# Performance work log

Measured on AMD Instinct MI355X. Metric: run time of the kernel, lower is better.

## Reference

```python
import jax, jax.numpy as jnp
import numpy as np

N_NODES = 50000
N_EDGES = 800000
F = 64
R = 32


def setup_inputs() -> dict:
    key = jax.random.key(0)
    ks = jax.random.split(key, 12)
    s = jax.random.normal(ks[0], (N_NODES, F), dtype=jnp.float32)
    v = jax.random.normal(ks[1], (N_NODES, 3, F), dtype=jnp.float32)
    radial_embeddings = jax.random.normal(ks[2], (N_EDGES, R), dtype=jnp.float32)
    f_cut = jax.random.uniform(ks[3], (N_EDGES,), dtype=jnp.float32)
    unit_vectors = jax.random.normal(ks[4], (N_EDGES, 3), dtype=jnp.float32)
    edge_index = jax.random.randint(ks[5], (2, N_EDGES), 0, N_NODES, dtype=jnp.int64 if jax.config.jax_enable_x64 else jnp.int32)
    # mlp_phi: Linear(F,F) -> SiLU -> Linear(F, 3F); linear_W: Linear(R, 3F)
    W1 = jax.random.normal(ks[6], (F, F), dtype=jnp.float32) / np.sqrt(F)
    b1 = jnp.zeros((F,), dtype=jnp.float32)
    W2 = jax.random.normal(ks[7], (F, 3 * F), dtype=jnp.float32) / np.sqrt(F)
    b2 = jnp.zeros((3 * F,), dtype=jnp.float32)
    Wr = jax.random.normal(ks[8], (R, 3 * F), dtype=jnp.float32) / np.sqrt(R)
    br = jnp.zeros((3 * F,), dtype=jnp.float32)
    return {"s": s, "v": v, "radial_embeddings": radial_embeddings, "f_cut": f_cut,
            "unit_vectors": unit_vectors, "edge_index": edge_index,
            "W1": W1, "b1": b1, "W2": W2, "b2": b2, "Wr": Wr, "br": br}


def reference(s, v, radial_embeddings, f_cut, unit_vectors, edge_index, W1, b1, W2, b2, Wr, br):
    idx_i, idx_j = edge_index[0], edge_index[1]
    n_nodes = s.shape[0]
    nf = s.shape[-1]
    # per-node MLP: Linear -> SiLU -> Linear to 3F channels
    phi = jax.nn.silu(s @ W1 + b1) @ W2 + b2            # [N, 3F]
    # radial filter weighted by cutoff
    W = (radial_embeddings @ Wr + br) * f_cut[:, None]   # [E, 3F]
    x = phi[idx_j] * W                                   # [E, 3F]  (gather + multiply)
    x_s, x_vv, x_vs = x[:, :nf], x[:, nf:2 * nf], x[:, 2 * nf:]
    ds = jax.ops.segment_sum(x_s, idx_i, num_segments=n_nodes)          # [N, F]
    x_v = v[idx_j] * x_vv[:, None, :] + x_vs[:, None, :] * unit_vectors[:, :, None]  # [E, 3, F]
    dv = jax.ops.segment_sum(x_v, idx_i, num_segments=n_nodes)          # [N, 3, F]
    return s + ds, v + dv
```

## Files before the change

kernel.cpp:

```cpp
#include <hip/hip_runtime.h>
#include <math.h>

#define N_NODES 50000
#define N_EDGES 800000
#define F 64
#define R 32
#define C3F 192
#define CAP 48
#define CSTRIDE 16
#define MLP_BLOCKS ((N_NODES + 31) / 32)
#define FILL_BLOCKS ((N_EDGES + 255) / 256)

#define REP32(X) X(0) X(1) X(2) X(3) X(4) X(5) X(6) X(7) \
                 X(8) X(9) X(10) X(11) X(12) X(13) X(14) X(15) \
                 X(16) X(17) X(18) X(19) X(20) X(21) X(22) X(23) \
                 X(24) X(25) X(26) X(27) X(28) X(29) X(30) X(31)

__global__ __launch_bounds__(256) void mlp_fill_kernel(
    const float* __restrict__ s, const float* __restrict__ W1,
    const float* __restrict__ b1, const float* __restrict__ W2,
    const float* __restrict__ b2, float* __restrict__ phi,
    const int* __restrict__ eidx, int* __restrict__ counts,
    int2* __restrict__ bucket)
{
    __shared__ float hid_s[32][68];

    if (blockIdx.x >= MLP_BLOCKS) {
        int e = (blockIdx.x - MLP_BLOCKS) * 256 + threadIdx.x;
        if (e < N_EDGES) {
            int i = eidx[e];
            int j = eidx[N_EDGES + e];
            int pos = atomicAdd(&counts[i * CSTRIDE], 1);
            if (pos < CAP) bucket[(size_t)i * CAP + pos] = make_int2(e, j);
        }
        return;
    }

    int n = threadIdx.x >> 3;
    int seg = threadIdx.x & 7;
    int node = blockIdx.x * 32 + n;
    bool live = node < N_NODES;

    if (live) {
        float sv[F];
        const float4* srow = (const float4*)(s + (size_t)node * F);
#pragma unroll
        for (int q = 0; q < F / 4; q++) {
            float4 t = srow[q];
            sv[4*q+0] = t.x; sv[4*q+1] = t.y; sv[4*q+2] = t.z; sv[4*q+3] = t.w;
        }
        float acc[8];
#pragma unroll
        for (int q = 0; q < 8; q++) acc[q] = b1[seg * 8 + q];
#pragma unroll
        for (int k = 0; k < F; k++) {
            float sk = sv[k];
            const float4* w = (const float4*)(W1 + (size_t)k * F + seg * 8);
            float4 w0 = w[0], w1 = w[1];
            acc[0] += sk * w0.x; acc[1] += sk * w0.y;
            acc[2] += sk * w0.z; acc[3] += sk * w0.w;
            acc[4] += sk * w1.x; acc[5] += sk * w1.y;
            acc[6] += sk * w1.z; acc[7] += sk * w1.w;
        }
#pragma unroll
        for (int q = 0; q < 8; q++) {
            float a = acc[q];
            hid_s[n][seg * 8 + q] = a / (1.f + __expf(-a));
        }
    }
    __syncthreads();

    if (!live) return;

    float hv[F];
#pragma unroll
    for (int q = 0; q < F; q++) hv[q] = hid_s[n][q];

    float acc[24];
#pragma unroll
    for (int q = 0; q < 24; q++) acc[q] = b2[seg * 24 + q];
#pragma unroll
    for (int k = 0; k < F; k++) {
        float hk = hv[k];
        const float4* w = (const float4*)(W2 + (size_t)k * C3F + seg * 24);
#pragma unroll
        for (int q4 = 0; q4 < 6; q4++) {
            float4 wv = w[q4];
            acc[q4*4+0] += hk * wv.x;
            acc[q4*4+1] += hk * wv.y;
            acc[q4*4+2] += hk * wv.z;
            acc[q4*4+3] += hk * wv.w;
        }
    }
    float4* o = (float4*)(phi + (size_t)node * C3F + seg * 24);
#pragma unroll
    for (int q4 = 0; q4 < 6; q4++)
        o[q4] = make_float4(acc[q4*4+0], acc[q4*4+1], acc[q4*4+2], acc[q4*4+3]);
}

__global__ __launch_bounds__(64, 4) void gather_kernel(
    const float* __restrict__ s, const float* __restrict__ v,
    const float* __restrict__ phi, const float* __restrict__ radial,
    const float* __restrict__ f_cut, const float* __restrict__ unit_vec,
    const float* __restrict__ Wr, const float* __restrict__ br,
    const int* __restrict__ counts, const int2* __restrict__ bucket,
    float* __restrict__ out_s, float* __restrict__ out_v)
{
    const int lane = threadIdx.x;
    const int node = blockIdx.x;

#define DECL_WR(r) float wrs##r, wrv##r, wrq##r;
    REP32(DECL_WR)
#undef DECL_WR
#define LOAD_WR(r) { const float* w_ = Wr + (r) * C3F; \
                     wrs##r = w_[lane]; wrv##r = w_[64 + lane]; \
                     wrq##r = w_[128 + lane]; }
    REP32(LOAD_WR)
#undef LOAD_WR
#define KA3(r) , "+v"(wrs##r), "+v"(wrv##r), "+v"(wrq##r)
    asm volatile("" : "+v"(wrs0) KA3(1) KA3(2) KA3(3) KA3(4) KA3(5) KA3(6) KA3(7), "+v"(wrv0), "+v"(wrq0));
    asm volatile("" : "+v"(wrs8) KA3(9) KA3(10) KA3(11) KA3(12) KA3(13) KA3(14) KA3(15), "+v"(wrv8), "+v"(wrq8));
    asm volatile("" : "+v"(wrs16) KA3(17) KA3(18) KA3(19) KA3(20) KA3(21) KA3(22) KA3(23), "+v"(wrv16), "+v"(wrq16));
    asm volatile("" : "+v"(wrs24) KA3(25) KA3(26) KA3(27) KA3(28) KA3(29) KA3(30) KA3(31), "+v"(wrv24), "+v"(wrq24));
#undef KA3

    const float b_s = br[lane], b_vv = br[64 + lane], b_vs = br[128 + lane];

    float acc_s = 0.f, acc_v0 = 0.f, acc_v1 = 0.f, acc_v2 = 0.f;

    int cnt = __builtin_amdgcn_readfirstlane(counts[node * CSTRIDE]);
    cnt = cnt < CAP ? cnt : CAP;
    const int2* row = bucket + (size_t)node * CAP;

    if (cnt > 0) {
        int2 ej0 = row[0];
        int e = __builtin_amdgcn_readfirstlane(ej0.x);
        int j = __builtin_amdgcn_readfirstlane(ej0.y);

        const float* pj = phi + (size_t)j * C3F;
        const float* vj = v + (size_t)j * C3F;
        float ps = pj[lane], pvv = pj[64 + lane], pvs = pj[128 + lane];
        float va = vj[lane], vb = vj[64 + lane], vc = vj[128 + lane];

        float fc = f_cut[e];
        float u0 = unit_vec[e * 3 + 0];
        float u1 = unit_vec[e * 3 + 1];
        float u2 = unit_vec[e * 3 + 2];
#define DECL_CR(r) float cr##r;
        REP32(DECL_CR)
#undef DECL_CR
        {
            const float* rp = radial + (size_t)e * R;
#define LOAD_CR(r) cr##r = rp[r];
            REP32(LOAD_CR)
#undef LOAD_CR
        }

        for (int k = 0; k < cnt; ++k) {
            int e_n = e, j_n = j;
            if (k + 1 < cnt) {
                int2 ejn = row[k + 1];
                e_n = __builtin_amdgcn_readfirstlane(ejn.x);
                j_n = __builtin_amdgcn_readfirstlane(ejn.y);
            }
            const float* pn = phi + (size_t)j_n * C3F;
            const float* vn = v + (size_t)j_n * C3F;
            float nps = pn[lane], npvv = pn[64 + lane], npvs = pn[128 + lane];
            float nva = vn[lane], nvb = vn[64 + lane], nvc = vn[128 + lane];
            float fc_n = f_cut[e_n];
            float nu0 = unit_vec[e_n * 3 + 0];
            float nu1 = unit_vec[e_n * 3 + 1];
            float nu2 = unit_vec[e_n * 3 + 2];
#define DECL_NR(r) float nr##r;
            REP32(DECL_NR)
#undef DECL_NR
            {
                const float* rpn = radial + (size_t)e_n * R;
#define LOAD_NR(r) nr##r = rpn[r];
                REP32(LOAD_NR)
#undef LOAD_NR
            }

            float ws = b_s, wvv = b_vv, wvs = b_vs;
#define FMA_WR(r) { ws  += cr##r * wrs##r; \
                    wvv += cr##r * wrv##r; \
                    wvs += cr##r * wrq##r; }
            REP32(FMA_WR)
#undef FMA_WR

            float xs  = ps  * ws  * fc;
            float xvv = pvv * wvv * fc;
            float xvs = pvs * wvs * fc;
            acc_s  += xs;
            acc_v0 += va * xvv + xvs * u0;
            acc_v1 += vb * xvv + xvs * u1;
            acc_v2 += vc * xvv + xvs * u2;

            e = e_n; j = j_n;
            ps = nps; pvv = npvv; pvs = npvs;
            va = nva; vb = nvb; vc = nvc;
            fc = fc_n; u0 = nu0; u1 = nu1; u2 = nu2;
#define ROT_R(r) cr##r = nr##r;
            REP32(ROT_R)
#undef ROT_R
        }
    }

    out_s[(size_t)node * F + lane] = s[(size_t)node * F + lane] + acc_s;
    const float* vi = v + (size_t)node * C3F;
    float* ovi = out_v + (size_t)node * C3F;
    ovi[lane]       = vi[lane]       + acc_v0;
    ovi[64 + lane]  = vi[64 + lane]  + acc_v1;
    ovi[128 + lane] = vi[128 + lane] + acc_v2;
}

extern "C" void kernel_launch(void* const* d_in, const int* in_sizes, int n_in,
                              void* d_out, int out_size, void* d_ws, size_t ws_size,
                              hipStream_t stream)
{
    const float* s      = (const float*)d_in[0];
    const float* v      = (const float*)d_in[1];
    const float* radial = (const float*)d_in[2];
    const float* f_cut  = (const float*)d_in[3];
    const float* unit   = (const float*)d_in[4];
    const int*   eidx   = (const int*)  d_in[5];
    const float* W1     = (const float*)d_in[6];
    const float* b1     = (const float*)d_in[7];
    const float* W2     = (const float*)d_in[8];
    const float* b2     = (const float*)d_in[9];
    const float* Wr     = (const float*)d_in[10];
    const float* br     = (const float*)d_in[11];

    float* out   = (float*)d_out;
    float* out_s = out;
    float* out_v = out + (size_t)N_NODES * F;

    float* phi    = (float*)d_ws;
    int*   counts = (int*)(phi + (size_t)N_NODES * C3F);
    int2*  bucket = (int2*)(counts + (size_t)N_NODES * CSTRIDE);

    hipMemsetAsync(counts, 0, (size_t)N_NODES * CSTRIDE * sizeof(int), stream);

    mlp_fill_kernel<<<MLP_BLOCKS + FILL_BLOCKS, 256, 0, stream>>>(
        s, W1, b1, W2, b2, phi, eidx, counts, bucket);

    gather_kernel<<<N_NODES, 64, 0, stream>>>(
        s, v, phi, radial, f_cut, unit, Wr, br,
        counts, bucket, out_s, out_v);
}
```

Before: 572.3 us.

## Split fused MLP/fill kernel, batch fill atomics per thread, split gather launch

```diff
diff --git a/kernel.cpp b/kernel.cpp
--- a/kernel.cpp
+++ b/kernel.cpp
@@ -9,32 +9,19 @@
 #define CAP 48
 #define CSTRIDE 16
 #define MLP_BLOCKS ((N_NODES + 31) / 32)
-#define FILL_BLOCKS ((N_EDGES + 255) / 256)
+#define FILL_BLOCKS ((N_EDGES + 1023) / 1024)
 
 #define REP32(X) X(0) X(1) X(2) X(3) X(4) X(5) X(6) X(7) \
                  X(8) X(9) X(10) X(11) X(12) X(13) X(14) X(15) \
                  X(16) X(17) X(18) X(19) X(20) X(21) X(22) X(23) \
                  X(24) X(25) X(26) X(27) X(28) X(29) X(30) X(31)
 
-__global__ __launch_bounds__(256) void mlp_fill_kernel(
+__global__ __launch_bounds__(256) void mlp_kernel(
     const float* __restrict__ s, const float* __restrict__ W1,
     const float* __restrict__ b1, const float* __restrict__ W2,
-    const float* __restrict__ b2, float* __restrict__ phi,
-    const int* __restrict__ eidx, int* __restrict__ counts,
-    int2* __restrict__ bucket)
+    const float* __restrict__ b2, float* __restrict__ phi)
 {
     __shared__ float hid_s[32][68];
-
-    if (blockIdx.x >= MLP_BLOCKS) {
-        int e = (blockIdx.x - MLP_BLOCKS) * 256 + threadIdx.x;
-        if (e < N_EDGES) {
-            int i = eidx[e];
-            int j = eidx[N_EDGES + e];
-            int pos = atomicAdd(&counts[i * CSTRIDE], 1);
-            if (pos < CAP) bucket[(size_t)i * CAP + pos] = make_int2(e, j);
-        }
-        return;
-    }
 
     int n = threadIdx.x >> 3;
     int seg = threadIdx.x & 7;
@@ -98,16 +85,42 @@
         o[q4] = make_float4(acc[q4*4+0], acc[q4*4+1], acc[q4*4+2], acc[q4*4+3]);
 }
 
+__global__ __launch_bounds__(256) void fill_kernel(
+    const int* __restrict__ eidx, int* __restrict__ counts,
+    int2* __restrict__ bucket)
+{
+    int base = blockIdx.x * 1024 + threadIdx.x;
+    int ii[4], jj[4];
+#pragma unroll
+    for (int q = 0; q < 4; q++) {
+        int e = base + q * 256;
+        ii[q] = -1;
+        if (e < N_EDGES) {
+            ii[q] = __builtin_nontemporal_load(&eidx[e]);
+            jj[q] = __builtin_nontemporal_load(&eidx[N_EDGES + e]);
+        }
+    }
+#pragma unroll
+    for (int q = 0; q < 4; q++) {
+        int e = base + q * 256;
+        if (ii[q] >= 0) {
+            int pos = atomicAdd(&counts[ii[q] * CSTRIDE], 1);
+            if (pos < CAP)
+                bucket[(size_t)ii[q] * CAP + pos] = make_int2(e, jj[q]);
+        }
+    }
+}
+
 __global__ __launch_bounds__(64, 4) void gather_kernel(
     const float* __restrict__ s, const float* __restrict__ v,
     const float* __restrict__ phi, const float* __restrict__ radial,
     const float* __restrict__ f_cut, const float* __restrict__ unit_vec,
     const float* __restrict__ Wr, const float* __restrict__ br,
     const int* __restrict__ counts, const int2* __restrict__ bucket,
-    float* __restrict__ out_s, float* __restrict__ out_v)
+    float* __restrict__ out_s, float* __restrict__ out_v, int node_base)
 {
     const int lane = threadIdx.x;
-    const int node = blockIdx.x;
+    const int node = node_base + blockIdx.x;
 
 #define DECL_WR(r) float wrs##r, wrv##r, wrq##r;
     REP32(DECL_WR)
@@ -241,10 +254,14 @@
 
     hipMemsetAsync(counts, 0, (size_t)N_NODES * CSTRIDE * sizeof(int), stream);
 
-    mlp_fill_kernel<<<MLP_BLOCKS + FILL_BLOCKS, 256, 0, stream>>>(
-        s, W1, b1, W2, b2, phi, eidx, counts, bucket);
-
-    gather_kernel<<<N_NODES, 64, 0, stream>>>(
+    fill_kernel<<<FILL_BLOCKS, 256, 0, stream>>>(eidx, counts, bucket);
+
+    mlp_kernel<<<MLP_BLOCKS, 256, 0, stream>>>(s, W1, b1, W2, b2, phi);
+
+    gather_kernel<<<N_NODES / 2, 64, 0, stream>>>(
         s, v, phi, radial, f_cut, unit, Wr, br,
-        counts, bucket, out_s, out_v);
-}
+        counts, bucket, out_s, out_v, 0);
+    gather_kernel<<<N_NODES / 2, 64, 0, stream>>>(
+        s, v, phi, radial, f_cut, unit, Wr, br,
+        counts, bucket, out_s, out_v, N_NODES / 2);
+}
```

Measured after the change: 624.9 us. 9.2% more time.
